# Optimization experiments

Hardware: AMD Instinct MI355X
Metric: run time of the kernel (lower is better)

Reference implementation:

```python
import jax, jax.numpy as jnp
import numpy as np

B, T, C = 2, 2048, 768
H, N_LEFT = 12, 6
D = C // H


def setup_inputs() -> dict:
    key = jax.random.key(0)
    ks = jax.random.split(key, 4)
    x = jax.random.normal(ks[0], (B, T, C), dtype=jnp.float32)
    attention_mask = jnp.ones((B, T), dtype=jnp.int32)
    Wqkv_w = jax.random.normal(ks[1], (3 * C, C), dtype=jnp.float32) * (C ** -0.5)
    Wqkv_b = jnp.zeros((3 * C,), dtype=jnp.float32)
    Wo_w = jax.random.normal(ks[2], (C, C), dtype=jnp.float32) * (C ** -0.5)
    Wo_b = jnp.zeros((C,), dtype=jnp.float32)
    return {"x": x, "attention_mask": attention_mask, "Wqkv_w": Wqkv_w,
            "Wqkv_b": Wqkv_b, "Wo_w": Wo_w, "Wo_b": Wo_b}


def _attend(q, k, v, mask):
    # q,k,v: [B,h,T,D]; mask: [B,1,T,T] additive
    s = jnp.einsum('bhqd,bhkd->bhqk', q, k) * (D ** -0.5) + mask
    a = jax.nn.softmax(s.astype(jnp.float32), axis=-1).astype(q.dtype)
    return jnp.einsum('bhqk,bhkd->bhqd', a, v)


def reference(x, attention_mask, Wqkv_w, Wqkv_b, Wo_w, Wo_b):
    neg = jnp.finfo(x.dtype).min
    # padding mask [B,1,1,T]: 0 where valid, neg where padded
    pad = (1.0 - attention_mask.astype(x.dtype))[:, None, None, :] * neg
    i = jnp.arange(T)
    tri = (i[None, :] > i[:, None]).astype(x.dtype) * neg   # triu(neg, 1)
    left_mask = tri[None, None] + pad                        # causal (look left)
    right_mask = tri.T[None, None] + pad                     # anti-causal (look right)

    qkv = (x @ Wqkv_w.T + Wqkv_b).reshape(B, T, 3, H, D)
    qkv = jnp.transpose(qkv, (0, 3, 2, 1, 4))                # [B,H,3,T,D]
    q, k, v = qkv[:, :, 0], qkv[:, :, 1], qkv[:, :, 2]

    lc = _attend(q[:, :N_LEFT], k[:, :N_LEFT], v[:, :N_LEFT], left_mask)
    rc = _attend(q[:, N_LEFT:], k[:, N_LEFT:], v[:, N_LEFT:], right_mask)
    ctx = jnp.concatenate([lc, rc], axis=1)                  # [B,H,T,D]
    ctx = jnp.transpose(ctx, (0, 2, 1, 3)).reshape(B, T, C)
    out = ctx @ Wo_w.T + Wo_b
    return out
```

## Files before the change

### kernel.cpp

```cpp
#include <hip/hip_runtime.h>


typedef unsigned short u16;
typedef __bf16 bf16x8 __attribute__((ext_vector_type(8)));
typedef float fx4 __attribute__((ext_vector_type(4)));
typedef unsigned short u16x8 __attribute__((ext_vector_type(8)));
typedef unsigned short u16x4 __attribute__((ext_vector_type(4)));
typedef _Float16 hx4 __attribute__((ext_vector_type(4)));
typedef __fp16 fp16x2 __attribute__((ext_vector_type(2)));

#define T_SEQ 2048
#define C_DIM 768
#define NHEAD 12
#define HDIM  64
#define NITEMS 768
#define LOG2E_8 0.18033688f

__device__ __forceinline__ u16 f2bf(float f) {
  unsigned u = __float_as_uint(f);
  u += 0x7fffu + ((u >> 16) & 1u);
  return (u16)(u >> 16);
}
__device__ __forceinline__ u16 f2h(float f) {
  union { _Float16 h; u16 u; } cv; cv.h = (_Float16)f; return cv.u;
}

__device__ __forceinline__ void gl2lds16(const u16* g, u16* l) {
  __builtin_amdgcn_global_load_lds(
      (const __attribute__((address_space(1))) void*)g,
      (__attribute__((address_space(3))) void*)l, 16, 0, 0);
}

__global__ void cvt_swz_k(const float* __restrict__ x,
                          const float* __restrict__ wqkv,
                          const float* __restrict__ wo,
                          u16* __restrict__ out) {
  int i = blockIdx.x * blockDim.x + threadIdx.x;
  if (i >= 688128) return;
  int m = i / 96;
  int c8 = (i - m * 96) << 3;
  const float* src;
  if (m < 4096)       src = x    + (size_t)m * C_DIM + c8;
  else if (m < 6400)  src = wqkv + (size_t)(m - 4096) * C_DIM + c8;
  else                src = wo   + (size_t)(m - 6400) * C_DIM + c8;
  fx4 a = *(const fx4*)src, b = *(const fx4*)(src + 4);
  u16x8 o;
  #pragma unroll
  for (int j = 0; j < 4; ++j) { o[j] = f2bf(a[j]); o[4 + j] = f2bf(b[j]); }
  *(u16x8*)&out[(size_t)m * C_DIM + (c8 ^ ((m & 7) << 3))] = o;
}

__global__ void maskcvt_k(const int* __restrict__ am, float* __restrict__ mf, int n) {
  int i = blockIdx.x * blockDim.x + threadIdx.x;
  if (i < n) mf[i] = am[i] ? 0.f : -1e30f;
}

__device__ __forceinline__ void gemm_core_64x128(const u16* __restrict__ A,
                                                 const u16* __restrict__ B,
                                                 int m0, int n0,
                                                 u16* As, u16* Bs,
                                                 fx4 acc[4][2]) {
  const int tid = threadIdx.x;
  const int lane = tid & 63, wv = tid >> 6;
  const int wn = wv << 5;
  const int lr = lane & 15, lg = lane >> 4;
  const int swk = (lr & 7) << 3;
  const int scol = (tid & 7) << 3;
  #pragma unroll
  for (int mt = 0; mt < 4; ++mt)
    #pragma unroll
    for (int nt = 0; nt < 2; ++nt) acc[mt][nt] = fx4{0.f, 0.f, 0.f, 0.f};

  for (int k0 = 0; k0 < C_DIM; k0 += 64) {
    __syncthreads();
    #pragma unroll
    for (int p = 0; p < 2; ++p) {
      int row = (tid + (p << 8)) >> 3;
      gl2lds16(&A[(size_t)(m0 + row) * C_DIM + k0 + scol], &As[(row << 6) + scol]);
    }
    #pragma unroll
    for (int p = 0; p < 4; ++p) {
      int row = (tid + (p << 8)) >> 3;
      gl2lds16(&B[(size_t)(n0 + row) * C_DIM + k0 + scol], &Bs[(row << 6) + scol]);
    }
    __syncthreads();
    #pragma unroll
    for (int kk = 0; kk < 64; kk += 32) {
      bf16x8 af[4], bfr[2];
      #pragma unroll
      for (int mt = 0; mt < 4; ++mt)
        af[mt] = *(const bf16x8*)&As[((mt * 16 + lr) << 6) + ((kk + lg * 8) ^ swk)];
      #pragma unroll
      for (int nt = 0; nt < 2; ++nt)
        bfr[nt] = *(const bf16x8*)&Bs[((wn + nt * 16 + lr) << 6) + ((kk + lg * 8) ^ swk)];
      #pragma unroll
      for (int mt = 0; mt < 4; ++mt)
        #pragma unroll
        for (int nt = 0; nt < 2; ++nt)
          acc[mt][nt] = __builtin_amdgcn_mfma_f32_16x16x32_bf16(
              af[mt], bfr[nt], acc[mt][nt], 0, 0, 0);
    }
  }
}

__global__ __launch_bounds__(256) void gemm_qkv_k(
    const u16* __restrict__ A, const u16* __restrict__ B,
    const float* __restrict__ bias,
    u16* __restrict__ qb, u16* __restrict__ kswz, u16* __restrict__ vswz) {
  __shared__ __align__(16) u16 As[64 * 64];
  __shared__ __align__(16) u16 Bs[128 * 64];
  int m0 = blockIdx.y << 6, n0 = blockIdx.x << 7;
  fx4 acc[4][2];
  gemm_core_64x128(A, B, m0, n0, As, Bs, acc);

  const int tid = threadIdx.x, lane = tid & 63, wv = tid >> 6;
  const int wn = wv << 5;
  const int lr = lane & 15, lg = lane >> 4;
  #pragma unroll
  for (int nt = 0; nt < 2; ++nt) {
    int n = n0 + wn + nt * 16 + lr;
    float bv = bias[n];
    int part = n / 768;
    int rem = n - part * 768;
    int h = rem >> 6, d = rem & 63;
    #pragma unroll
    for (int mt = 0; mt < 4; ++mt) {
      #pragma unroll
      for (int r = 0; r < 4; ++r) {
        int m = m0 + mt * 16 + lg * 4 + r;
        int bb = m >> 11, t = m & 2047;
        int bh = bb * NHEAD + h;
        int kt = t >> 6, tr = t & 63;
        float val = acc[mt][nt][r] + bv;
        if (part == 0) {
          qb[(((size_t)bh << 11) + t) * HDIM + d] = f2bf(val);
        } else if (part == 1) {
          kswz[((size_t)(bh * 32 + kt) << 12) + (tr << 6) + (d ^ ((tr & 7) << 3))] =
              f2bf(val);
        } else {
          vswz[((size_t)(bh * 32 + kt) << 12) + (d << 6) + (tr ^ ((d & 15) << 2))] =
              f2h(val);
        }
      }
    }
  }
}

__device__ __forceinline__ void gemm_core_64x64(const u16* __restrict__ A,
                                                const u16* __restrict__ B,
                                                int m0, int n0,
                                                u16* As, u16* Bs,
                                                fx4 acc[2][2]) {
  const int tid = threadIdx.x;
  const int lane = tid & 63, wv = tid >> 6;
  const int wm = (wv & 1) << 5, wn = (wv >> 1) << 5;
  const int lr = lane & 15, lg = lane >> 4;
  const int swk = (lr & 7) << 3;
  const int scol = (tid & 7) << 3;
  #pragma unroll
  for (int mt = 0; mt < 2; ++mt)
    #pragma unroll
    for (int nt = 0; nt < 2; ++nt) acc[mt][nt] = fx4{0.f, 0.f, 0.f, 0.f};

  for (int k0 = 0; k0 < C_DIM; k0 += 64) {
    __syncthreads();
    #pragma unroll
    for (int p = 0; p < 2; ++p) {
      int row = (tid + (p << 8)) >> 3;
      gl2lds16(&A[(size_t)(m0 + row) * C_DIM + k0 + scol], &As[(row << 6) + scol]);
      gl2lds16(&B[(size_t)(n0 + row) * C_DIM + k0 + scol], &Bs[(row << 6) + scol]);
    }
    __syncthreads();
    #pragma unroll
    for (int kk = 0; kk < 64; kk += 32) {
      bf16x8 af[2], bfr[2];
      #pragma unroll
      for (int mt = 0; mt < 2; ++mt)
        af[mt] = *(const bf16x8*)&As[((wm + mt * 16 + lr) << 6) + ((kk + lg * 8) ^ swk)];
      #pragma unroll
      for (int nt = 0; nt < 2; ++nt)
        bfr[nt] = *(const bf16x8*)&Bs[((wn + nt * 16 + lr) << 6) + ((kk + lg * 8) ^ swk)];
      #pragma unroll
      for (int mt = 0; mt < 2; ++mt)
        #pragma unroll
        for (int nt = 0; nt < 2; ++nt)
          acc[mt][nt] = __builtin_amdgcn_mfma_f32_16x16x32_bf16(
              af[mt], bfr[nt], acc[mt][nt], 0, 0, 0);
    }
  }
}

__global__ __launch_bounds__(256) void gemm_out_k(
    const u16* __restrict__ A, const u16* __restrict__ B,
    const float* __restrict__ bias, float* __restrict__ out) {
  __shared__ __align__(16) u16 As[64 * 64];
  __shared__ __align__(16) u16 Bs[64 * 64];
  int m0 = blockIdx.y << 6, n0 = blockIdx.x << 6;
  fx4 acc[2][2];
  gemm_core_64x64(A, B, m0, n0, As, Bs, acc);

  const int tid = threadIdx.x, lane = tid & 63, wv = tid >> 6;
  const int wm = (wv & 1) << 5, wn = (wv >> 1) << 5;
  const int lr = lane & 15, lg = lane >> 4;
  #pragma unroll
  for (int nt = 0; nt < 2; ++nt) {
    int n = n0 + wn + nt * 16 + lr;
    float bv = bias[n];
    #pragma unroll
    for (int mt = 0; mt < 2; ++mt) {
      #pragma unroll
      for (int r = 0; r < 4; ++r) {
        int m = m0 + wm + mt * 16 + lg * 4 + r;
        out[(size_t)m * C_DIM + n] = acc[mt][nt][r] + bv;
      }
    }
  }
}

__global__ __launch_bounds__(256) void attn_k(
    const u16* __restrict__ q, const u16* __restrict__ kswz,
    const u16* __restrict__ vswz, const float* __restrict__ maskf,
    u16* __restrict__ ctx, int* __restrict__ counter) {
  __shared__ __align__(16) u16 Ks[2][4096];
  __shared__ __align__(16) u16 Vt[2][4096];
  __shared__ int s_w;

  const int tid = threadIdx.x, lane = tid & 63, wv = tid >> 6;
  const int lr = lane & 15, lg = lane >> 4;
  const int swk = (lr & 7) << 3;
  const int swv = (lr & 15) << 2;

  for (;;) {
    if (tid == 0) s_w = atomicAdd(counter, 1);
    __syncthreads();
    int w = s_w;
    if (w >= NITEMS) break;
    int qslot = w / 24, bh = w - qslot * 24;
    int bb = bh / NHEAD, h = bh - bb * NHEAD;
    bool causal = (h < 6);
    int qt = causal ? (31 - qslot) : qslot;
    int kt0 = causal ? 0 : qt;
    int kt1 = causal ? qt : 31;
    size_t tile_base = (size_t)(bh * 32) << 12;

    {
      const u16* kg = kswz + tile_base + ((size_t)kt0 << 12);
      const u16* vg = vswz + tile_base + ((size_t)kt0 << 12);
      #pragma unroll
      for (int c2 = 0; c2 < 2; ++c2) {
        int e = (wv << 10) + (c2 << 9) + (lane << 3);
        gl2lds16(kg + e, &Ks[0][e]);
        gl2lds16(vg + e, &Vt[0][e]);
      }
    }

    int q0 = qt << 6;
    size_t head_off = ((size_t)bh << 11) * HDIM;
    int qrow = q0 + wv * 16 + lr;
    bf16x8 qf0 = *(const bf16x8*)&q[head_off + (size_t)qrow * HDIM + lg * 8];
    bf16x8 qf1 = *(const bf16x8*)&q[head_off + (size_t)qrow * HDIM + 32 + lg * 8];
    const float* mrow = maskf + (bb << 11);

    fx4 o[4];
    #pragma unroll
    for (int dt = 0; dt < 4; ++dt) o[dt] = fx4{0.f, 0.f, 0.f, 0.f};
    float l_i = 0.f;

    int buf = 0;
    for (int kt = kt0; kt <= kt1; ++kt, buf ^= 1) {
      __syncthreads();
      if (kt < kt1) {
        const u16* kg = kswz + tile_base + ((size_t)(kt + 1) << 12);
        const u16* vg = vswz + tile_base + ((size_t)(kt + 1) << 12);
        #pragma unroll
        for (int c2 = 0; c2 < 2; ++c2) {
          int e = (wv << 10) + (c2 << 9) + (lane << 3);
          gl2lds16(kg + e, &Ks[buf ^ 1][e]);
          gl2lds16(vg + e, &Vt[buf ^ 1][e]);
        }
      }

      fx4 st[4];
      #pragma unroll
      for (int nt = 0; nt < 4; ++nt) {
        const u16* kr = &Ks[buf][(nt * 16 + lr) << 6];
        bf16x8 kf0 = *(const bf16x8*)&kr[(lg * 8) ^ swk];
        bf16x8 kf1 = *(const bf16x8*)&kr[(32 + lg * 8) ^ swk];
        fx4 z = fx4{0.f, 0.f, 0.f, 0.f};
        z = __builtin_amdgcn_mfma_f32_16x16x32_bf16(kf0, qf0, z, 0, 0, 0);
        st[nt] = __builtin_amdgcn_mfma_f32_16x16x32_bf16(kf1, qf1, z, 0, 0, 0);
      }

      float psum = 0.f;
      if (kt == qt) {
        #pragma unroll
        for (int nt = 0; nt < 4; ++nt) {
          int kb0 = (kt << 6) + nt * 16 + lg * 4;
          fx4 mv = *(const fx4*)&mrow[kb0];
          #pragma unroll
          for (int r = 0; r < 4; ++r) {
            float arg = st[nt][r] * LOG2E_8 + mv[r];
            int kabs = kb0 + r;
            bool dead = causal ? (kabs > qrow) : (kabs < qrow);
            arg = dead ? -1e30f : arg;
            float p = __builtin_amdgcn_exp2f(arg);
            st[nt][r] = p;
            psum += p;
          }
        }
      } else {
        #pragma unroll
        for (int nt = 0; nt < 4; ++nt) {
          int kb0 = (kt << 6) + nt * 16 + lg * 4;
          fx4 mv = *(const fx4*)&mrow[kb0];
          #pragma unroll
          for (int r = 0; r < 4; ++r) {
            float p = __builtin_amdgcn_exp2f(st[nt][r] * LOG2E_8 + mv[r]);
            st[nt][r] = p;
            psum += p;
          }
        }
      }
      l_i += psum;

      #pragma unroll
      for (int nt = 0; nt < 4; ++nt) {
        union { hx4 v; fp16x2 h[2]; } pu;
        pu.h[0] = __builtin_amdgcn_cvt_pkrtz(st[nt][0], st[nt][1]);
        pu.h[1] = __builtin_amdgcn_cvt_pkrtz(st[nt][2], st[nt][3]);
        hx4 pf = pu.v;
        #pragma unroll
        for (int dt = 0; dt < 4; ++dt) {
          const u16* vr = &Vt[buf][(dt * 16 + lr) << 6];
          hx4 vf = *(const hx4*)&vr[(nt * 16 + lg * 4) ^ swv];
          o[dt] = __builtin_amdgcn_mfma_f32_16x16x16f16(vf, pf, o[dt], 0, 0, 0);
        }
      }
    }

    l_i += __shfl_xor(l_i, 16, 64);
    l_i += __shfl_xor(l_i, 32, 64);
    float inv = 1.f / l_i;
    size_t rowb = ((size_t)(bb << 11) + qrow) * C_DIM;
    int csw = (qrow & 7) << 3;
    #pragma unroll
    for (int dt = 0; dt < 4; ++dt) {
      u16x4 pk;
      #pragma unroll
      for (int r = 0; r < 4; ++r) pk[r] = f2bf(o[dt][r] * inv);
      int colb = h * HDIM + dt * 16 + lg * 4;
      *(u16x4*)&ctx[rowb + (colb ^ csw)] = pk;
    }
  }
}

extern "C" void kernel_launch(void* const* d_in, const int* in_sizes, int n_in,
                              void* d_out, int out_size, void* d_ws, size_t ws_size,
                              hipStream_t stream) {
  const float* x     = (const float*)d_in[0];
  const int*   amask = (const int*)d_in[1];
  const float* wqkv  = (const float*)d_in[2];
  const float* bqkv  = (const float*)d_in[3];
  const float* wo    = (const float*)d_in[4];
  const float* bo    = (const float*)d_in[5];
  float* out = (float*)d_out;

  char* ws = (char*)d_ws;
  u16*   xb    = (u16*)(ws + 0);
  u16*   wqkvb = (u16*)(ws + 6291456);
  u16*   wob   = (u16*)(ws + 9830400);
  u16*   qb    = (u16*)(ws + 11010048);
  u16*   kswz  = (u16*)(ws + 17301504);
  u16*   vswz  = (u16*)(ws + 23592960);
  u16*   ctxb  = (u16*)(ws + 29884416);
  float* maskf = (float*)(ws + 36175872);
  int*   cnt   = (int*)(ws + 36192256);

  cvt_swz_k<<<2688, 256, 0, stream>>>(x, wqkv, wo, xb);
  maskcvt_k<<<16, 256, 0, stream>>>(amask, maskf, 4096);
  (void)hipMemsetAsync(cnt, 0, 4, stream);

  gemm_qkv_k<<<dim3(18, 64), 256, 0, stream>>>(xb, wqkvb, bqkv, qb, kswz, vswz);
  attn_k<<<512, 256, 0, stream>>>(qb, kswz, vswz, maskf, ctxb, cnt);
  gemm_out_k<<<dim3(12, 64), 256, 0, stream>>>(ctxb, wob, bo, out);
}
```

Baseline: 170.7 us.

## Double-buffer LDS in both GEMMs and stage V epilogue through LDS

Both projection GEMM cores now use two LDS buffers. The next K-tile is issued into the spare buffer while MFMAs run on the current one, which removes one barrier per K iteration and hides global load latency. The QKV kernel's V-part epilogue now writes fp16 values into LDS first and then stores them to the swizzled V layout as 8-byte vectors, replacing scattered 2-byte stores. The cost is double the LDS per block, which may lower occupancy, and correctness relies on the async loads having landed by the next barrier.

```diff
diff --git a/kernel.cpp b/kernel.cpp
--- a/kernel.cpp
+++ b/kernel.cpp
@@ -71,28 +71,45 @@
     #pragma unroll
     for (int nt = 0; nt < 2; ++nt) acc[mt][nt] = fx4{0.f, 0.f, 0.f, 0.f};
 
-  for (int k0 = 0; k0 < C_DIM; k0 += 64) {
+  #pragma unroll
+  for (int p = 0; p < 2; ++p) {
+    int row = (tid >> 3) + (p << 5);
+    gl2lds16(&A[(size_t)(m0 + row) * C_DIM + scol], &As[(row << 6) + scol]);
+  }
+  #pragma unroll
+  for (int p = 0; p < 4; ++p) {
+    int row = (tid >> 3) + (p << 5);
+    gl2lds16(&B[(size_t)(n0 + row) * C_DIM + scol], &Bs[(row << 6) + scol]);
+  }
+
+  int buf = 0;
+  for (int k0 = 0; k0 < C_DIM; k0 += 64, buf ^= 1) {
     __syncthreads();
-    #pragma unroll
-    for (int p = 0; p < 2; ++p) {
-      int row = (tid + (p << 8)) >> 3;
-      gl2lds16(&A[(size_t)(m0 + row) * C_DIM + k0 + scol], &As[(row << 6) + scol]);
-    }
-    #pragma unroll
-    for (int p = 0; p < 4; ++p) {
-      int row = (tid + (p << 8)) >> 3;
-      gl2lds16(&B[(size_t)(n0 + row) * C_DIM + k0 + scol], &Bs[(row << 6) + scol]);
-    }
-    __syncthreads();
+    if (k0 + 64 < C_DIM) {
+      u16* Ad = &As[(buf ^ 1) << 12];
+      u16* Bd = &Bs[(buf ^ 1) << 13];
+      #pragma unroll
+      for (int p = 0; p < 2; ++p) {
+        int row = (tid >> 3) + (p << 5);
+        gl2lds16(&A[(size_t)(m0 + row) * C_DIM + k0 + 64 + scol], &Ad[(row << 6) + scol]);
+      }
+      #pragma unroll
+      for (int p = 0; p < 4; ++p) {
+        int row = (tid >> 3) + (p << 5);
+        gl2lds16(&B[(size_t)(n0 + row) * C_DIM + k0 + 64 + scol], &Bd[(row << 6) + scol]);
+      }
+    }
+    const u16* Ab = &As[buf << 12];
+    const u16* Bb = &Bs[buf << 13];
     #pragma unroll
     for (int kk = 0; kk < 64; kk += 32) {
       bf16x8 af[4], bfr[2];
       #pragma unroll
       for (int mt = 0; mt < 4; ++mt)
-        af[mt] = *(const bf16x8*)&As[((mt * 16 + lr) << 6) + ((kk + lg * 8) ^ swk)];
+        af[mt] = *(const bf16x8*)&Ab[((mt * 16 + lr) << 6) + ((kk + lg * 8) ^ swk)];
       #pragma unroll
       for (int nt = 0; nt < 2; ++nt)
-        bfr[nt] = *(const bf16x8*)&Bs[((wn + nt * 16 + lr) << 6) + ((kk + lg * 8) ^ swk)];
+        bfr[nt] = *(const bf16x8*)&Bb[((wn + nt * 16 + lr) << 6) + ((kk + lg * 8) ^ swk)];
       #pragma unroll
       for (int mt = 0; mt < 4; ++mt)
         #pragma unroll
@@ -107,41 +124,68 @@
     const u16* __restrict__ A, const u16* __restrict__ B,
     const float* __restrict__ bias,
     u16* __restrict__ qb, u16* __restrict__ kswz, u16* __restrict__ vswz) {
-  __shared__ __align__(16) u16 As[64 * 64];
-  __shared__ __align__(16) u16 Bs[128 * 64];
+  __shared__ __align__(16) u16 As[2][64 * 64];
+  __shared__ __align__(16) u16 Bs[2][128 * 64];
   int m0 = blockIdx.y << 6, n0 = blockIdx.x << 7;
   fx4 acc[4][2];
-  gemm_core_64x128(A, B, m0, n0, As, Bs, acc);
+  gemm_core_64x128(A, B, m0, n0, &As[0][0], &Bs[0][0], acc);
 
   const int tid = threadIdx.x, lane = tid & 63, wv = tid >> 6;
   const int wn = wv << 5;
   const int lr = lane & 15, lg = lane >> 4;
-  #pragma unroll
-  for (int nt = 0; nt < 2; ++nt) {
-    int n = n0 + wn + nt * 16 + lr;
-    float bv = bias[n];
-    int part = n / 768;
-    int rem = n - part * 768;
-    int h = rem >> 6, d = rem & 63;
-    #pragma unroll
-    for (int mt = 0; mt < 4; ++mt) {
-      #pragma unroll
-      for (int r = 0; r < 4; ++r) {
-        int m = m0 + mt * 16 + lg * 4 + r;
-        int bb = m >> 11, t = m & 2047;
-        int bh = bb * NHEAD + h;
-        int kt = t >> 6, tr = t & 63;
-        float val = acc[mt][nt][r] + bv;
-        if (part == 0) {
-          qb[(((size_t)bh << 11) + t) * HDIM + d] = f2bf(val);
-        } else if (part == 1) {
-          kswz[((size_t)(bh * 32 + kt) << 12) + (tr << 6) + (d ^ ((tr & 7) << 3))] =
-              f2bf(val);
-        } else {
-          vswz[((size_t)(bh * 32 + kt) << 12) + (d << 6) + (tr ^ ((d & 15) << 2))] =
-              f2h(val);
+  const int part = n0 / 768;
+
+  if (part < 2) {
+    #pragma unroll
+    for (int nt = 0; nt < 2; ++nt) {
+      int n = n0 + wn + nt * 16 + lr;
+      float bv = bias[n];
+      int rem = n - part * 768;
+      int h = rem >> 6, d = rem & 63;
+      #pragma unroll
+      for (int mt = 0; mt < 4; ++mt) {
+        #pragma unroll
+        for (int r = 0; r < 4; ++r) {
+          int m = m0 + mt * 16 + lg * 4 + r;
+          int bb = m >> 11, t = m & 2047;
+          int bh = bb * NHEAD + h;
+          int kt = t >> 6, tr = t & 63;
+          float val = acc[mt][nt][r] + bv;
+          if (part == 0)
+            qb[(((size_t)bh << 11) + t) * HDIM + d] = f2bf(val);
+          else
+            kswz[((size_t)(bh * 32 + kt) << 12) + (tr << 6) + (d ^ ((tr & 7) << 3))] =
+                f2bf(val);
         }
       }
+    }
+  } else {
+    u16* Vs = &Bs[0][0];
+    __syncthreads();
+    #pragma unroll
+    for (int nt = 0; nt < 2; ++nt) {
+      int n_local = wn + nt * 16 + lr;
+      float bv = bias[n0 + n_local];
+      #pragma unroll
+      for (int mt = 0; mt < 4; ++mt) {
+        u16x4 pk;
+        #pragma unroll
+        for (int r = 0; r < 4; ++r) pk[r] = f2h(acc[mt][nt][r] + bv);
+        int m4 = (mt << 2) + lg;
+        *(u16x4*)&Vs[(n_local << 6) + ((m4 ^ (n_local & 15)) << 2)] = pk;
+      }
+    }
+    __syncthreads();
+    int bb = m0 >> 11, kt = (m0 >> 6) & 31;
+    int tr4 = tid & 15;
+    #pragma unroll
+    for (int p = 0; p < 8; ++p) {
+      int n_local = (tid >> 4) + (p << 4);
+      int nglob = n0 - 1536 + n_local;
+      int h = nglob >> 6, d = nglob & 63;
+      u16x4 v = *(const u16x4*)&Vs[(n_local << 6) + ((tr4 ^ (n_local & 15)) << 2)];
+      size_t tile = (size_t)((bb * NHEAD + h) * 32 + kt) << 12;
+      *(u16x4*)&vswz[tile + (d << 6) + ((tr4 ^ (d & 15)) << 2)] = v;
     }
   }
 }
@@ -162,24 +206,37 @@
     #pragma unroll
     for (int nt = 0; nt < 2; ++nt) acc[mt][nt] = fx4{0.f, 0.f, 0.f, 0.f};
 
-  for (int k0 = 0; k0 < C_DIM; k0 += 64) {
+  #pragma unroll
+  for (int p = 0; p < 2; ++p) {
+    int row = (tid >> 3) + (p << 5);
+    gl2lds16(&A[(size_t)(m0 + row) * C_DIM + scol], &As[(row << 6) + scol]);
+    gl2lds16(&B[(size_t)(n0 + row) * C_DIM + scol], &Bs[(row << 6) + scol]);
+  }
+
+  int buf = 0;
+  for (int k0 = 0; k0 < C_DIM; k0 += 64, buf ^= 1) {
     __syncthreads();
-    #pragma unroll
-    for (int p = 0; p < 2; ++p) {
-      int row = (tid + (p << 8)) >> 3;
-      gl2lds16(&A[(size_t)(m0 + row) * C_DIM + k0 + scol], &As[(row << 6) + scol]);
-      gl2lds16(&B[(size_t)(n0 + row) * C_DIM + k0 + scol], &Bs[(row << 6) + scol]);
-    }
-    __syncthreads();
+    if (k0 + 64 < C_DIM) {
+      u16* Ad = &As[(buf ^ 1) << 12];
+      u16* Bd = &Bs[(buf ^ 1) << 12];
+      #pragma unroll
+      for (int p = 0; p < 2; ++p) {
+        int row = (tid >> 3) + (p << 5);
+        gl2lds16(&A[(size_t)(m0 + row) * C_DIM + k0 + 64 + scol], &Ad[(row << 6) + scol]);
+        gl2lds16(&B[(size_t)(n0 + row) * C_DIM + k0 + 64 + scol], &Bd[(row << 6) + scol]);
+      }
+    }
+    const u16* Ab = &As[buf << 12];
+    const u16* Bb = &Bs[buf << 12];
     #pragma unroll
     for (int kk = 0; kk < 64; kk += 32) {
       bf16x8 af[2], bfr[2];
       #pragma unroll
       for (int mt = 0; mt < 2; ++mt)
-        af[mt] = *(const bf16x8*)&As[((wm + mt * 16 + lr) << 6) + ((kk + lg * 8) ^ swk)];
+        af[mt] = *(const bf16x8*)&Ab[((wm + mt * 16 + lr) << 6) + ((kk + lg * 8) ^ swk)];
       #pragma unroll
       for (int nt = 0; nt < 2; ++nt)
-        bfr[nt] = *(const bf16x8*)&Bs[((wn + nt * 16 + lr) << 6) + ((kk + lg * 8) ^ swk)];
+        bfr[nt] = *(const bf16x8*)&Bb[((wn + nt * 16 + lr) << 6) + ((kk + lg * 8) ^ swk)];
       #pragma unroll
       for (int mt = 0; mt < 2; ++mt)
         #pragma unroll
@@ -193,11 +250,11 @@
 __global__ __launch_bounds__(256) void gemm_out_k(
     const u16* __restrict__ A, const u16* __restrict__ B,
     const float* __restrict__ bias, float* __restrict__ out) {
-  __shared__ __align__(16) u16 As[64 * 64];
-  __shared__ __align__(16) u16 Bs[64 * 64];
+  __shared__ __align__(16) u16 As[2][64 * 64];
+  __shared__ __align__(16) u16 Bs[2][64 * 64];
   int m0 = blockIdx.y << 6, n0 = blockIdx.x << 6;
   fx4 acc[2][2];
-  gemm_core_64x64(A, B, m0, n0, As, Bs, acc);
+  gemm_core_64x64(A, B, m0, n0, &As[0][0], &Bs[0][0], acc);
 
   const int tid = threadIdx.x, lane = tid & 63, wv = tid >> 6;
   const int wm = (wv & 1) << 5, wn = (wv >> 1) << 5;
```

New measurement: 174.2 us. 1.02x slower.
